# Optimization experiments

Hardware: AMD Instinct MI355X
Metric: run time of the kernel (lower is better)

The kernel has to match this reference:

```python
import jax, jax.numpy as jnp
import numpy as np

NUM_NODES = 100000
NUM_REL_P1 = 238  # num_relations + 1 (extra column for self-connection relation id -1)
B = 32768
S = 16
D_IN = 256
D_OUT = 256


def setup_inputs() -> dict:
    key = jax.random.key(0)
    k1, k2, k3, k4, k5 = jax.random.split(key, 5)
    neighbors = jax.random.randint(k1, (B, S), 0, NUM_NODES)          # sampled neighbor node ids
    relations = jax.random.randint(k2, (B, S), 0, NUM_REL_P1)          # sampled relation ids
    features = jax.random.normal(k3, (NUM_NODES, D_IN), dtype=jnp.float32)
    weight = jax.random.normal(k4, (D_OUT, D_IN), dtype=jnp.float32) * (1.0 / np.sqrt(D_IN))
    relation_weight = jax.random.normal(k5, (D_OUT, NUM_REL_P1), dtype=jnp.float32) * 0.05
    return {"neighbors": neighbors, "relations": relations, "features": features,
            "weight": weight, "relation_weight": relation_weight}


def reference(neighbors, relations, features, weight, relation_weight):
    # gather sampled neighbor embeddings: [B, S, D_in]
    neighbor_emb = features[neighbors]
    # mean-aggregate over the sample dim: [B, D_in]
    agg_neighbors = neighbor_emb.mean(axis=1)
    # linear transform: [B, D_in] @ [D_in, D_out] -> [B, D_out]
    agg_neighbors = agg_neighbors @ weight.T
    # gather + mean relation embeddings: [B, S, D_out] -> [B, D_out]
    agg_relations = relation_weight.T[relations].mean(axis=1)
    return jax.nn.relu(agg_neighbors + agg_relations)
```

## Files before the change

### kernel.cpp

```cpp
#include <hip/hip_runtime.h>

#define B_ROWS  32768
#define S_SAMP  16
#define NRELS   238
#define DIM     256
#define N_NODES 100000
#define NF4     ((N_NODES * DIM) / 4)
#define CONV_BLOCKS (NF4 / 256)

typedef __attribute__((ext_vector_type(8))) short  short8;
typedef __attribute__((ext_vector_type(8))) unsigned short ushort8;
typedef __attribute__((ext_vector_type(4))) float  f32x4;

static __device__ __forceinline__ unsigned short f2bf(float f) {
    unsigned int u = __float_as_uint(f);
    u += 0x7FFFu + ((u >> 16) & 1u);
    return (unsigned short)(u >> 16);
}
static __device__ __forceinline__ float bf2f(unsigned short u) {
    return __uint_as_float(((unsigned int)u) << 16);
}

__global__ __launch_bounds__(256) void prep_kernel(const float* __restrict__ F,
                                                   const float* __restrict__ W,
                                                   const float* __restrict__ RW,
                                                   unsigned short* __restrict__ Fb,
                                                   unsigned short* __restrict__ Wb,
                                                   unsigned short* __restrict__ RWb) {
    if (blockIdx.x < CONV_BLOCKS) {
        int i = blockIdx.x * 256 + threadIdx.x;
        float4 v = ((const float4*)F)[i];
        ushort4 p;
        p.x = f2bf(v.x); p.y = f2bf(v.y); p.z = f2bf(v.z); p.w = f2bf(v.w);
        ((ushort4*)Fb)[i] = p;
    } else {
        int i = (blockIdx.x - CONV_BLOCKS) * 256 + threadIdx.x;
        if (i < DIM * DIM) {
            Wb[i] = f2bf(W[i]);
            int n = i >> 8;
            int k = i & 255;
            RWb[i] = (k < NRELS) ? f2bf(RW[n * NRELS + k]) : (unsigned short)0;
        }
    }
}

__global__ __launch_bounds__(256, 4) void fused_kernel(const int* __restrict__ nbr,
                                                       const int* __restrict__ rels,
                                                       const unsigned short* __restrict__ Fb,
                                                       const unsigned short* __restrict__ RWb,
                                                       const unsigned short* __restrict__ Wb,
                                                       float* __restrict__ out) {
    __shared__ unsigned short As[32][264];
    __shared__ unsigned short Cs[32][264];
    __shared__ unsigned int   cnt4[32][32];
    const int tid  = threadIdx.x;
    const int lane = tid & 63;
    const int wid  = __builtin_amdgcn_readfirstlane(tid >> 6);
    const int half = lane >> 5;
    const int li   = lane & 31;
    const int col0 = lane & 15;
    const int quad = lane >> 4;
    const int r0g  = blockIdx.x * 32;

    unsigned int* c4 = (unsigned int*)cnt4;
    c4[tid] = 0u; c4[tid + 256] = 0u; c4[tid + 512] = 0u; c4[tid + 768] = 0u;
    __syncthreads();

    {
        const int hr = tid >> 3;
        const int hs = tid & 7;
        int rid0 = rels[(r0g + hr) * S_SAMP + hs];
        int rid1 = rels[(r0g + hr) * S_SAMP + hs + 8];
        atomicAdd(&cnt4[hr][rid0 >> 3], 1u << ((rid0 & 7) * 4));
        atomicAdd(&cnt4[hr][rid1 >> 3], 1u << ((rid1 & 7) * 4));
    }

    const float sc = 1.0f / 16.0f;
    for (int i = 0; i < 8; ++i) {
        const int row_l = wid * 8 + i;
        const int row_g = r0g + row_l;
        const int2* nb2 = (const int2*)(nbr + row_g * S_SAMP);
        float af[8] = {0.f, 0.f, 0.f, 0.f, 0.f, 0.f, 0.f, 0.f};
#pragma unroll
        for (int t = 0; t < 8; ++t) {
            int2 nn = nb2[t];
            int nid = half ? nn.y : nn.x;
            ushort8 f = *(const ushort8*)(Fb + (size_t)nid * DIM + li * 8);
#pragma unroll
            for (int j = 0; j < 8; ++j) af[j] += bf2f(f[j]);
        }
        ushort8 pk;
#pragma unroll
        for (int j = 0; j < 8; ++j) {
            float full = af[j] + __shfl_xor(af[j], 32, 64);
            pk[j] = f2bf(full * sc);
        }
        if (!half) *(ushort8*)&As[row_l][li * 8] = pk;
    }

    short8 Breg[4][4];
#pragma unroll
    for (int j = 0; j < 4; ++j)
#pragma unroll
        for (int kk = 0; kk < 4; ++kk)
            Breg[j][kk] = *(const short8*)(Wb + (size_t)((wid * 4 + j) * 16 + col0) * DIM
                                              + kk * 32 + quad * 8);
    __syncthreads();

    {
        const int rr = tid >> 3;
        const int kb = (tid & 7) * 32;
#pragma unroll
        for (int g = 0; g < 4; ++g) {
            unsigned int w = cnt4[rr][(kb >> 3) + g];
            ushort8 ck;
#pragma unroll
            for (int j = 0; j < 8; ++j)
                ck[j] = f2bf((float)((w >> (4 * j)) & 0xFu) * 0.0625f);
            *(ushort8*)&Cs[rr][kb + g * 8] = ck;
        }
    }
    __syncthreads();

    f32x4 acc[2][4];
#pragma unroll
    for (int mt = 0; mt < 2; ++mt)
#pragma unroll
        for (int j = 0; j < 4; ++j) acc[mt][j] = (f32x4){0.f, 0.f, 0.f, 0.f};

#pragma unroll
    for (int mt = 0; mt < 2; ++mt) {
        const int mrow = mt * 16 + col0;
#pragma unroll
        for (int kk = 0; kk < 4; ++kk) {
            short8 a = *(const short8*)&As[mrow][kk * 32 + quad * 8];
#pragma unroll
            for (int j = 0; j < 4; ++j)
                acc[mt][j] = __builtin_amdgcn_mfma_f32_16x16x32_bf16(a, Breg[j][kk], acc[mt][j], 0, 0, 0);
        }
    }
#pragma unroll
    for (int j = 0; j < 4; ++j)
#pragma unroll
        for (int kk = 0; kk < 4; ++kk)
            Breg[j][kk] = *(const short8*)(Wb + (size_t)((wid * 4 + j) * 16 + col0) * DIM
                                              + (kk + 4) * 32 + quad * 8);
#pragma unroll
    for (int mt = 0; mt < 2; ++mt) {
        const int mrow = mt * 16 + col0;
#pragma unroll
        for (int kk = 0; kk < 4; ++kk) {
            short8 a = *(const short8*)&As[mrow][(kk + 4) * 32 + quad * 8];
#pragma unroll
            for (int j = 0; j < 4; ++j)
                acc[mt][j] = __builtin_amdgcn_mfma_f32_16x16x32_bf16(a, Breg[j][kk], acc[mt][j], 0, 0, 0);
        }
    }
#pragma unroll
    for (int j = 0; j < 4; ++j)
#pragma unroll
        for (int kk = 0; kk < 4; ++kk)
            Breg[j][kk] = *(const short8*)(RWb + (size_t)((wid * 4 + j) * 16 + col0) * DIM
                                               + kk * 32 + quad * 8);
#pragma unroll
    for (int mt = 0; mt < 2; ++mt) {
        const int mrow = mt * 16 + col0;
#pragma unroll
        for (int kk = 0; kk < 4; ++kk) {
            short8 a = *(const short8*)&Cs[mrow][kk * 32 + quad * 8];
#pragma unroll
            for (int j = 0; j < 4; ++j)
                acc[mt][j] = __builtin_amdgcn_mfma_f32_16x16x32_bf16(a, Breg[j][kk], acc[mt][j], 0, 0, 0);
        }
    }
#pragma unroll
    for (int j = 0; j < 4; ++j)
#pragma unroll
        for (int kk = 0; kk < 4; ++kk)
            Breg[j][kk] = *(const short8*)(RWb + (size_t)((wid * 4 + j) * 16 + col0) * DIM
                                               + (kk + 4) * 32 + quad * 8);
#pragma unroll
    for (int mt = 0; mt < 2; ++mt) {
        const int mrow = mt * 16 + col0;
#pragma unroll
        for (int kk = 0; kk < 4; ++kk) {
            short8 a = *(const short8*)&Cs[mrow][(kk + 4) * 32 + quad * 8];
#pragma unroll
            for (int j = 0; j < 4; ++j)
                acc[mt][j] = __builtin_amdgcn_mfma_f32_16x16x32_bf16(a, Breg[j][kk], acc[mt][j], 0, 0, 0);
        }
    }

#pragma unroll
    for (int mt = 0; mt < 2; ++mt) {
#pragma unroll
        for (int j = 0; j < 4; ++j) {
            const int col = (wid * 4 + j) * 16 + col0;
#pragma unroll
            for (int i2 = 0; i2 < 4; ++i2) {
                const int r_l = mt * 16 + quad * 4 + i2;
                float v = acc[mt][j][i2];
                out[(size_t)(r0g + r_l) * DIM + col] = v > 0.f ? v : 0.f;
            }
        }
    }
}

extern "C" void kernel_launch(void* const* d_in, const int* in_sizes, int n_in,
                              void* d_out, int out_size, void* d_ws, size_t ws_size,
                              hipStream_t stream) {
    const int*   neighbors = (const int*)d_in[0];
    const int*   relations = (const int*)d_in[1];
    const float* features  = (const float*)d_in[2];
    const float* weight    = (const float*)d_in[3];
    const float* relw      = (const float*)d_in[4];
    float* out = (float*)d_out;

    char* ws = (char*)d_ws;
    unsigned short* Wb  = (unsigned short*)ws;
    unsigned short* RWb = (unsigned short*)(ws + 131072);
    unsigned short* Fb  = (unsigned short*)(ws + 262144);

    prep_kernel<<<CONV_BLOCKS + 256, 256, 0, stream>>>(features, weight, relw, Fb, Wb, RWb);
    fused_kernel<<<B_ROWS / 32, 256, 0, stream>>>(neighbors, relations, Fb, RWb, Wb, out);
}
```

Before: 225.8 us.

## Split fused block across 8 waves with smaller per-wave tiles

Doubles the block to 512 threads so each wave gathers 4 rows instead of 8 and computes 32 output columns instead of 64. The two weight GEMMs are merged into one loop that loads smaller B fragments per k-chunk. The aim is more waves in flight to hide gather latency and lower register pressure. The trade-off is losing the early prefetch of W fragments before the barrier, plus more barrier participants per block.

```diff
diff --git a/kernel.cpp b/kernel.cpp
--- a/kernel.cpp
+++ b/kernel.cpp
@@ -44,7 +44,7 @@
     }
 }
 
-__global__ __launch_bounds__(256, 4) void fused_kernel(const int* __restrict__ nbr,
+__global__ __launch_bounds__(512, 8) void fused_kernel(const int* __restrict__ nbr,
                                                        const int* __restrict__ rels,
                                                        const unsigned short* __restrict__ Fb,
                                                        const unsigned short* __restrict__ RWb,
@@ -63,21 +63,17 @@
     const int r0g  = blockIdx.x * 32;
 
     unsigned int* c4 = (unsigned int*)cnt4;
-    c4[tid] = 0u; c4[tid + 256] = 0u; c4[tid + 512] = 0u; c4[tid + 768] = 0u;
+    c4[tid] = 0u; c4[tid + 512] = 0u;
     __syncthreads();
 
     {
-        const int hr = tid >> 3;
-        const int hs = tid & 7;
-        int rid0 = rels[(r0g + hr) * S_SAMP + hs];
-        int rid1 = rels[(r0g + hr) * S_SAMP + hs + 8];
-        atomicAdd(&cnt4[hr][rid0 >> 3], 1u << ((rid0 & 7) * 4));
-        atomicAdd(&cnt4[hr][rid1 >> 3], 1u << ((rid1 & 7) * 4));
+        int rid = rels[r0g * S_SAMP + tid];
+        atomicAdd(&cnt4[tid >> 4][rid >> 3], 1u << ((rid & 7) * 4));
     }
 
     const float sc = 1.0f / 16.0f;
-    for (int i = 0; i < 8; ++i) {
-        const int row_l = wid * 8 + i;
+    for (int i = 0; i < 4; ++i) {
+        const int row_l = wid * 4 + i;
         const int row_g = r0g + row_l;
         const int2* nb2 = (const int2*)(nbr + row_g * S_SAMP);
         float af[8] = {0.f, 0.f, 0.f, 0.f, 0.f, 0.f, 0.f, 0.f};
@@ -97,105 +93,62 @@
         }
         if (!half) *(ushort8*)&As[row_l][li * 8] = pk;
     }
-
-    short8 Breg[4][4];
-#pragma unroll
-    for (int j = 0; j < 4; ++j)
-#pragma unroll
-        for (int kk = 0; kk < 4; ++kk)
-            Breg[j][kk] = *(const short8*)(Wb + (size_t)((wid * 4 + j) * 16 + col0) * DIM
-                                              + kk * 32 + quad * 8);
     __syncthreads();
 
     {
-        const int rr = tid >> 3;
-        const int kb = (tid & 7) * 32;
+        const int rr = tid >> 4;
+        const int w2 = tid & 15;
 #pragma unroll
-        for (int g = 0; g < 4; ++g) {
-            unsigned int w = cnt4[rr][(kb >> 3) + g];
+        for (int g = 0; g < 2; ++g) {
+            unsigned int w = cnt4[rr][w2 * 2 + g];
             ushort8 ck;
 #pragma unroll
             for (int j = 0; j < 8; ++j)
                 ck[j] = f2bf((float)((w >> (4 * j)) & 0xFu) * 0.0625f);
-            *(ushort8*)&Cs[rr][kb + g * 8] = ck;
+            *(ushort8*)&Cs[rr][(w2 * 2 + g) * 8] = ck;
         }
     }
     __syncthreads();
 
-    f32x4 acc[2][4];
+    f32x4 acc[2][2];
 #pragma unroll
     for (int mt = 0; mt < 2; ++mt)
 #pragma unroll
-        for (int j = 0; j < 4; ++j) acc[mt][j] = (f32x4){0.f, 0.f, 0.f, 0.f};
+        for (int j = 0; j < 2; ++j) acc[mt][j] = (f32x4){0.f, 0.f, 0.f, 0.f};
 
 #pragma unroll
-    for (int mt = 0; mt < 2; ++mt) {
-        const int mrow = mt * 16 + col0;
+    for (int s = 0; s < 2; ++s) {
+        const unsigned short* Bp = s ? RWb : Wb;
 #pragma unroll
-        for (int kk = 0; kk < 4; ++kk) {
-            short8 a = *(const short8*)&As[mrow][kk * 32 + quad * 8];
+        for (int kh = 0; kh < 4; ++kh) {
+            short8 Breg[2][2];
 #pragma unroll
-            for (int j = 0; j < 4; ++j)
-                acc[mt][j] = __builtin_amdgcn_mfma_f32_16x16x32_bf16(a, Breg[j][kk], acc[mt][j], 0, 0, 0);
-        }
-    }
+            for (int j = 0; j < 2; ++j)
 #pragma unroll
-    for (int j = 0; j < 4; ++j)
+                for (int kk = 0; kk < 2; ++kk)
+                    Breg[j][kk] = *(const short8*)(Bp + (size_t)((wid * 2 + j) * 16 + col0) * DIM
+                                                      + (kh * 2 + kk) * 32 + quad * 8);
 #pragma unroll
-        for (int kk = 0; kk < 4; ++kk)
-            Breg[j][kk] = *(const short8*)(Wb + (size_t)((wid * 4 + j) * 16 + col0) * DIM
-                                              + (kk + 4) * 32 + quad * 8);
+            for (int mt = 0; mt < 2; ++mt) {
+                const int mrow = mt * 16 + col0;
 #pragma unroll
-    for (int mt = 0; mt < 2; ++mt) {
-        const int mrow = mt * 16 + col0;
+                for (int kk = 0; kk < 2; ++kk) {
+                    short8 a;
+                    if (s == 0) a = *(const short8*)&As[mrow][(kh * 2 + kk) * 32 + quad * 8];
+                    else        a = *(const short8*)&Cs[mrow][(kh * 2 + kk) * 32 + quad * 8];
 #pragma unroll
-        for (int kk = 0; kk < 4; ++kk) {
-            short8 a = *(const short8*)&As[mrow][(kk + 4) * 32 + quad * 8];
-#pragma unroll
-            for (int j = 0; j < 4; ++j)
-                acc[mt][j] = __builtin_amdgcn_mfma_f32_16x16x32_bf16(a, Breg[j][kk], acc[mt][j], 0, 0, 0);
-        }
-    }
-#pragma unroll
-    for (int j = 0; j < 4; ++j)
-#pragma unroll
-        for (int kk = 0; kk < 4; ++kk)
-            Breg[j][kk] = *(const short8*)(RWb + (size_t)((wid * 4 + j) * 16 + col0) * DIM
-                                               + kk * 32 + quad * 8);
-#pragma unroll
-    for (int mt = 0; mt < 2; ++mt) {
-        const int mrow = mt * 16 + col0;
-#pragma unroll
-        for (int kk = 0; kk < 4; ++kk) {
-            short8 a = *(const short8*)&Cs[mrow][kk * 32 + quad * 8];
-#pragma unroll
-            for (int j = 0; j < 4; ++j)
-                acc[mt][j] = __builtin_amdgcn_mfma_f32_16x16x32_bf16(a, Breg[j][kk], acc[mt][j], 0, 0, 0);
-        }
-    }
-#pragma unroll
-    for (int j = 0; j < 4; ++j)
-#pragma unroll
-        for (int kk = 0; kk < 4; ++kk)
-            Breg[j][kk] = *(const short8*)(RWb + (size_t)((wid * 4 + j) * 16 + col0) * DIM
-                                               + (kk + 4) * 32 + quad * 8);
-#pragma unroll
-    for (int mt = 0; mt < 2; ++mt) {
-        const int mrow = mt * 16 + col0;
-#pragma unroll
-        for (int kk = 0; kk < 4; ++kk) {
-            short8 a = *(const short8*)&Cs[mrow][(kk + 4) * 32 + quad * 8];
-#pragma unroll
-            for (int j = 0; j < 4; ++j)
-                acc[mt][j] = __builtin_amdgcn_mfma_f32_16x16x32_bf16(a, Breg[j][kk], acc[mt][j], 0, 0, 0);
+                    for (int j = 0; j < 2; ++j)
+                        acc[mt][j] = __builtin_amdgcn_mfma_f32_16x16x32_bf16(a, Breg[j][kk], acc[mt][j], 0, 0, 0);
+                }
+            }
         }
     }
 
 #pragma unroll
     for (int mt = 0; mt < 2; ++mt) {
 #pragma unroll
-        for (int j = 0; j < 4; ++j) {
-            const int col = (wid * 4 + j) * 16 + col0;
+        for (int j = 0; j < 2; ++j) {
+            const int col = (wid * 2 + j) * 16 + col0;
 #pragma unroll
             for (int i2 = 0; i2 < 4; ++i2) {
                 const int r_l = mt * 16 + quad * 4 + i2;
@@ -222,5 +175,5 @@
     unsigned short* Fb  = (unsigned short*)(ws + 262144);
 
     prep_kernel<<<CONV_BLOCKS + 256, 256, 0, stream>>>(features, weight, relw, Fb, Wb, RWb);
-    fused_kernel<<<B_ROWS / 32, 256, 0, stream>>>(neighbors, relations, Fb, RWb, Wb, out);
+    fused_kernel<<<B_ROWS / 32, 512, 0, stream>>>(neighbors, relations, Fb, RWb, Wb, out);
 }
```

After: 224.3 us. Within noise of the previous version (-0.7%).
